# Optimization experiments

Hardware: AMD Instinct MI355X
Metric: run time of the kernel (lower is better)

Reference implementation:

```python
import jax, jax.numpy as jnp
import numpy as np

N_USERS = 100000
N_MOVIES = 20000
E = 2_000_000
D = 64          # in_units
F = 4           # num_factor
C = 5           # num_classes
H = 64          # hidden width of the edge MLP


def setup_inputs() -> dict:
    key = jax.random.key(0)
    ks = jax.random.split(key, 7)
    return {
        "ufeat": jax.random.normal(ks[0], (N_USERS, D), dtype=jnp.float32),
        "ifeat": jax.random.normal(ks[1], (N_MOVIES, D), dtype=jnp.float32),
        "W1": jax.random.normal(ks[2], (2 * D, H), dtype=jnp.float32) * 0.05,
        "W2": jax.random.normal(ks[3], (H, H), dtype=jnp.float32) * 0.05,
        "Wp": jax.random.normal(ks[4], (H, C), dtype=jnp.float32) * 0.05,
        "src_idx": jax.random.randint(ks[5], (E,), 0, N_USERS, dtype=jnp.int64) if jax.config.jax_enable_x64 else jax.random.randint(ks[5], (E,), 0, N_USERS, dtype=jnp.int32),
        "dst_idx": jax.random.randint(ks[6], (E,), 0, N_MOVIES, dtype=jnp.int32),
    }


def reference(ufeat, ifeat, W1, W2, Wp, src_idx, dst_idx):
    # Gather per-edge endpoint features (irregular access)
    h_u = ufeat[src_idx]   # [E, D]
    h_v = ifeat[dst_idx]   # [E, D]
    d = D // F
    # num_factor > 1 path: per-factor concat [h_u_k, h_v_k], then flatten.
    # Equivalent vectorized form: interleave factor blocks of u and v.
    x = jnp.concatenate(
        [h_u.reshape(-1, F, d), h_v.reshape(-1, F, d)], axis=2
    ).reshape(-1, 2 * D)   # [E, 2D]
    # Bias-free MLP: Linear -> exact GELU -> Linear (dropout rate is 0.0)
    h_fea = jax.nn.gelu(x @ W1, approximate=False) @ W2   # [E, 64]
    score = h_fea @ Wp                                    # [E, C] (squeeze is a no-op for C>1)
    return score, h_fea
```

## Files before the change

### kernel.cpp

```cpp
#include <hip/hip_runtime.h>
#include <hip/hip_bf16.h>

typedef short bf16x8 __attribute__((ext_vector_type(8)));
typedef float f32x4 __attribute__((ext_vector_type(4)));

#define E_TOTAL 2000000
#define MT 64
#define NTILES (E_TOTAL / MT)
#define NBLK (NTILES / 2)

#define NU 100000
#define NV 20000
#define NBU ((NU + 63) / 64)
#define NBV ((NV + 63) / 64)

#define OFF_W1UG 0
#define OFF_W1VG 4096
#define OFF_B2G  8192
#define OFF_U1   16384
#define OFF_V1   (16384 + 6400000)
#define WS_NEEDED_BYTES ((size_t)(OFF_V1 + 1280000) * 2)

#define FB_XP 136
#define FB_GP 72

__device__ __forceinline__ unsigned short f2bf(float x) {
  __hip_bfloat16 h = __float2bfloat16(x);
  return __builtin_bit_cast(unsigned short, h);
}
__device__ __forceinline__ float bf2f(unsigned short u) {
  unsigned int v = ((unsigned int)u) << 16;
  return __builtin_bit_cast(float, v);
}
__device__ __forceinline__ float gelu_exact(float x) {
  return 0.5f * x * (1.0f + erff(x * 0.70710678118654752f));
}
__device__ __forceinline__ float gelu_fast(float x) {
  float x2 = x * x;
  float inner = __builtin_fmaf(0.044715f * x, x2, x);
  float e = __builtin_amdgcn_exp2f(inner * 2.3022081f);
  float r = __builtin_amdgcn_rcpf(e + 1.0f);
  return __builtin_fmaf(-x, r, x);
}

__global__ void prep_w(const float* __restrict__ W1, const float* __restrict__ W2,
                       const float* __restrict__ Wp, unsigned short* __restrict__ ws) {
  int t = blockIdx.x * blockDim.x + threadIdx.x;
  int stride = gridDim.x * blockDim.x;
  unsigned short* W1ug = ws + OFF_W1UG;
  unsigned short* W1vg = ws + OFF_W1VG;
  unsigned short* B2g  = ws + OFF_B2G;
  for (int i = t; i < 4096; i += stride) {
    int n = i >> 6, k = i & 63;
    int xc = 32 * (k >> 4) + (k & 15);
    W1ug[i] = f2bf(W1[xc * 64 + n]);
    W1vg[i] = f2bf(W1[(xc + 16) * 64 + n]);
  }
  for (int i = t; i < 80 * 64; i += stride) {
    int n = i >> 6, k = i & 63;
    float v;
    if (n < 64) {
      v = W2[k * 64 + n];
    } else if (n < 69) {
      int c = n - 64;
      float s = 0.f;
      for (int j = 0; j < 64; ++j) s += W2[k * 64 + j] * Wp[j * 5 + c];
      v = s;
    } else {
      v = 0.f;
    }
    B2g[i] = f2bf(v);
  }
}

__global__ __launch_bounds__(256)
void prep_uv(const float* __restrict__ ufeat, const float* __restrict__ ifeat,
             const unsigned short* __restrict__ ws, unsigned short* __restrict__ wsmut) {
  const bool isU = (blockIdx.x < NBU);
  const int rows0 = (isU ? blockIdx.x : blockIdx.x - NBU) * 64;
  const int nrows = isU ? NU : NV;
  const float* feat = isU ? ufeat : ifeat;
  const unsigned short* Wg = ws + (isU ? OFF_W1UG : OFF_W1VG);
  unsigned short* outp = wsmut + (isU ? OFF_U1 : OFF_V1);

  const int lane = threadIdx.x & 63;
  const int w    = threadIdx.x >> 6;
  const int lr   = lane & 15;
  const int q    = lane >> 4;

  int row = rows0 + w * 16 + lr;
  int rowc = row < nrows ? row : nrows - 1;

  const f32x4 fz = {0.f, 0.f, 0.f, 0.f};
  f32x4 acc[4] = {fz, fz, fz, fz};
  #pragma unroll
  for (int kk = 0; kk < 2; ++kk) {
    int k0 = kk * 32 + q * 8;
    float4 fa = *reinterpret_cast<const float4*>(feat + (size_t)rowc * 64 + k0);
    float4 fb = *reinterpret_cast<const float4*>(feat + (size_t)rowc * 64 + k0 + 4);
    bf16x8 a;
    a[0] = (short)f2bf(fa.x); a[1] = (short)f2bf(fa.y);
    a[2] = (short)f2bf(fa.z); a[3] = (short)f2bf(fa.w);
    a[4] = (short)f2bf(fb.x); a[5] = (short)f2bf(fb.y);
    a[6] = (short)f2bf(fb.z); a[7] = (short)f2bf(fb.w);
    #pragma unroll
    for (int nt = 0; nt < 4; ++nt) {
      bf16x8 b = *reinterpret_cast<const bf16x8*>(&Wg[(nt * 16 + lr) * 64 + k0]);
      acc[nt] = __builtin_amdgcn_mfma_f32_16x16x32_bf16(b, a, acc[nt], 0, 0, 0);
    }
  }
  if (row < nrows) {
    #pragma unroll
    for (int nt = 0; nt < 4; ++nt) {
      ushort4 p;
      p.x = f2bf(acc[nt][0]); p.y = f2bf(acc[nt][1]);
      p.z = f2bf(acc[nt][2]); p.w = f2bf(acc[nt][3]);
      *reinterpret_cast<ushort4*>(&outp[(size_t)row * 64 + nt * 16 + 4 * q]) = p;
    }
  }
}

__device__ __forceinline__ void tile_compute(
    const unsigned short* __restrict__ B2g,
    bf16x8 u0, bf16x8 u1, bf16x8 v0, bf16x8 v1,
    int tbase, int w, int lr, int q, float* __restrict__ out) {
  const f32x4 fz = {0.f, 0.f, 0.f, 0.f};
  f32x4 acc[5] = {fz, fz, fz, fz, fz};
  bf16x8 g0, g1;
  #pragma unroll
  for (int e = 0; e < 8; ++e) {
    float x = bf2f((unsigned short)u0[e]) + bf2f((unsigned short)v0[e]);
    g0[e] = (short)f2bf(gelu_fast(x));
  }
  #pragma unroll
  for (int e = 0; e < 8; ++e) {
    float y = bf2f((unsigned short)u1[e]) + bf2f((unsigned short)v1[e]);
    g1[e] = (short)f2bf(gelu_fast(y));
  }
  const int k0 = q * 8;
  #pragma unroll
  for (int nt = 0; nt < 5; ++nt) {
    bf16x8 b0 = *reinterpret_cast<const bf16x8*>(&B2g[(nt * 16 + lr) * 64 + k0]);
    bf16x8 b1 = *reinterpret_cast<const bf16x8*>(&B2g[(nt * 16 + lr) * 64 + 32 + k0]);
    acc[nt] = __builtin_amdgcn_mfma_f32_16x16x32_bf16(b0, g0, acc[nt], 0, 0, 0);
    acc[nt] = __builtin_amdgcn_mfma_f32_16x16x32_bf16(b1, g1, acc[nt], 0, 0, 0);
  }
  float* out_score = out;
  float* out_h     = out + 10000000;
  const size_t edge = (size_t)(tbase + w * 16 + lr);
  #pragma unroll
  for (int nt = 0; nt < 4; ++nt)
    __builtin_nontemporal_store(acc[nt],
        reinterpret_cast<f32x4*>(&out_h[edge * 64 + nt * 16 + 4 * q]));
  if (q == 0) {
    *reinterpret_cast<f32x4*>(&out_score[edge * 5]) = acc[4];
  } else if (q == 1) {
    out_score[edge * 5 + 4] = acc[4][0];
  }
}

__global__ __launch_bounds__(256, 5)
void mlp_main5(const unsigned short* __restrict__ ws,
               const int* __restrict__ src, const int* __restrict__ dst,
               float* __restrict__ out) {
  const unsigned short* U1  = ws + OFF_U1;
  const unsigned short* V1  = ws + OFF_V1;
  const unsigned short* B2g = ws + OFF_B2G;

  const int lane = threadIdx.x & 63;
  const int w    = threadIdx.x >> 6;
  const int lr   = lane & 15;
  const int q    = lane >> 4;

  const int tb = blockIdx.x * (2 * MT);
  const int eA = tb + w * 16 + lr;
  const int eB = eA + 64;

  const int iA0 = src[eA];
  const int iA1 = dst[eA];
  const int iB0 = src[eB];
  const int iB1 = dst[eB];

  const unsigned short* upA = U1 + (size_t)iA0 * 64 + q * 8;
  const unsigned short* vpA = V1 + (size_t)iA1 * 64 + q * 8;
  const unsigned short* upB = U1 + (size_t)iB0 * 64 + q * 8;
  const unsigned short* vpB = V1 + (size_t)iB1 * 64 + q * 8;

  bf16x8 uA0 = *reinterpret_cast<const bf16x8*>(upA);
  bf16x8 uA1 = *reinterpret_cast<const bf16x8*>(upA + 32);
  bf16x8 vA0 = *reinterpret_cast<const bf16x8*>(vpA);
  bf16x8 vA1 = *reinterpret_cast<const bf16x8*>(vpA + 32);
  bf16x8 uB0 = *reinterpret_cast<const bf16x8*>(upB);
  bf16x8 uB1 = *reinterpret_cast<const bf16x8*>(upB + 32);
  bf16x8 vB0 = *reinterpret_cast<const bf16x8*>(vpB);
  bf16x8 vB1 = *reinterpret_cast<const bf16x8*>(vpB + 32);

  tile_compute(B2g, uA0, uA1, vA0, vA1, tb,      w, lr, q, out);
  tile_compute(B2g, uB0, uB1, vB0, vB1, tb + 64, w, lr, q, out);
}

__global__ void prep_kernel_fb(const float* __restrict__ W1, const float* __restrict__ W2,
                               const float* __restrict__ Wp,
                               unsigned short* __restrict__ W1g,
                               unsigned short* __restrict__ B2g) {
  int t = blockIdx.x * blockDim.x + threadIdx.x;
  int stride = gridDim.x * blockDim.x;
  for (int i = t; i < 64 * 128; i += stride) {
    int n = i >> 7, k = i & 127;
    W1g[i] = f2bf(W1[k * 64 + n]);
  }
  for (int i = t; i < 80 * 64; i += stride) {
    int n = i >> 6, k = i & 63;
    float v;
    if (n < 64) v = W2[k * 64 + n];
    else if (n < 69) {
      int c = n - 64; float s = 0.f;
      for (int j = 0; j < 64; ++j) s += W2[k * 64 + j] * Wp[j * 5 + c];
      v = s;
    } else v = 0.f;
    B2g[i] = f2bf(v);
  }
}

__global__ __launch_bounds__(256, 8)
void mlp_main_fb(const float* __restrict__ ufeat, const float* __restrict__ ifeat,
                 const int* __restrict__ src, const int* __restrict__ dst,
                 const unsigned short* __restrict__ W1g, const unsigned short* __restrict__ B2g,
                 float* __restrict__ out) {
  __shared__ __align__(16) unsigned short Xb[MT * FB_XP];
  const int lid  = threadIdx.x;
  const int lane = lid & 63;
  const int w    = lid >> 6;
  const int lr   = lane & 15;
  const int q    = lane >> 4;
  const int lk   = q << 3;
  const int tbase = blockIdx.x * MT;
  const int c  = lid & 15;
  const int rb = lid >> 4;
  int eidx[8];
  #pragma unroll
  for (int j = 0; j < 8; ++j) {
    int r = rb + 16 * j;
    eidx[j] = (r < 64) ? src[tbase + r] : dst[tbase + r - 64];
  }
  #pragma unroll
  for (int j = 0; j < 8; ++j) {
    int r = rb + 16 * j;
    int half = r >> 6;
    int e = r & 63;
    const float* base = (half ? ifeat : ufeat) + (size_t)eidx[j] * 64 + c * 4;
    float4 f = *reinterpret_cast<const float4*>(base);
    int col = ((c >> 2) * 32) + half * 16 + ((c & 3) * 4);
    ushort4 p;
    p.x = f2bf(f.x); p.y = f2bf(f.y); p.z = f2bf(f.z); p.w = f2bf(f.w);
    *reinterpret_cast<ushort4*>(&Xb[e * FB_XP + col]) = p;
  }
  __syncthreads();
  const f32x4 fz = {0.f, 0.f, 0.f, 0.f};
  f32x4 acc1[4] = {fz, fz, fz, fz};
  {
    const unsigned short* Xr = &Xb[(w * 16 + lr) * FB_XP];
    #pragma unroll
    for (int kk = 0; kk < 4; ++kk) {
      int ko = kk * 32 + lk;
      bf16x8 a = *reinterpret_cast<const bf16x8*>(Xr + ko);
      #pragma unroll
      for (int nt = 0; nt < 4; ++nt) {
        bf16x8 b = *reinterpret_cast<const bf16x8*>(&W1g[(nt * 16 + lr) * 128 + ko]);
        acc1[nt] = __builtin_amdgcn_mfma_f32_16x16x32_bf16(a, b, acc1[nt], 0, 0, 0);
      }
    }
  }
  __syncthreads();
  unsigned short* g = Xb;
  #pragma unroll
  for (int nt = 0; nt < 4; ++nt) {
    f32x4 v = acc1[nt];
    #pragma unroll
    for (int r = 0; r < 4; ++r)
      g[(w * 16 + 4 * q + r) * FB_GP + nt * 16 + lr] = f2bf(gelu_exact(v[r]));
  }
  __syncthreads();
  f32x4 acc2[5] = {fz, fz, fz, fz, fz};
  #pragma unroll
  for (int kk = 0; kk < 2; ++kk) {
    int ko = kk * 32 + lk;
    bf16x8 a = *reinterpret_cast<const bf16x8*>(&g[(w * 16 + lr) * FB_GP + ko]);
    #pragma unroll
    for (int nt = 0; nt < 5; ++nt) {
      bf16x8 b = *reinterpret_cast<const bf16x8*>(&B2g[(nt * 16 + lr) * 64 + ko]);
      acc2[nt] = __builtin_amdgcn_mfma_f32_16x16x32_bf16(a, b, acc2[nt], 0, 0, 0);
    }
  }
  float* out_score = out;
  float* out_h     = out + 10000000;
  {
    int er0 = tbase + w * 16 + 4 * q;
    #pragma unroll
    for (int nt = 0; nt < 4; ++nt) {
      #pragma unroll
      for (int r = 0; r < 4; ++r)
        out_h[(size_t)(er0 + r) * 64 + nt * 16 + lr] = acc2[nt][r];
    }
    if (lr < 5) {
      #pragma unroll
      for (int r = 0; r < 4; ++r)
        out_score[(size_t)(er0 + r) * 5 + lr] = acc2[4][r];
    }
  }
}

extern "C" void kernel_launch(void* const* d_in, const int* in_sizes, int n_in,
                              void* d_out, int out_size, void* d_ws, size_t ws_size,
                              hipStream_t stream) {
  const float* ufeat = (const float*)d_in[0];
  const float* ifeat = (const float*)d_in[1];
  const float* W1    = (const float*)d_in[2];
  const float* W2    = (const float*)d_in[3];
  const float* Wp    = (const float*)d_in[4];
  const int*   src   = (const int*)d_in[5];
  const int*   dst   = (const int*)d_in[6];

  unsigned short* ws = (unsigned short*)d_ws;

  if (ws_size >= WS_NEEDED_BYTES) {
    prep_w<<<16, 256, 0, stream>>>(W1, W2, Wp, ws);
    prep_uv<<<NBU + NBV, 256, 0, stream>>>(ufeat, ifeat, ws, ws);
    mlp_main5<<<NBLK, 256, 0, stream>>>(ws, src, dst, (float*)d_out);
  } else {
    unsigned short* W1g = ws;
    unsigned short* B2g = ws + 8192;
    prep_kernel_fb<<<16, 256, 0, stream>>>(W1, W2, Wp, W1g, B2g);
    mlp_main_fb<<<NTILES, 256, 0, stream>>>(ufeat, ifeat, src, dst, W1g, B2g, (float*)d_out);
  }
}
```

Measured before the change: 191.1 us.

## Convert main kernel to persistent grid with software-pipelined gathers

Replaces the one-shot kernel, where each block handles two tiles, with a persistent grid of 1024 blocks that loop over tiles in a grid stride. Each block keeps the W2/Wp weight fragments in registers and prefetches indices two tiles ahead and gathered features one tile ahead, so gather latency overlaps with GELU, MFMA and stores. The occupancy hint drops from 5 to 4 to make room for the extra live registers. With fewer waves resident, there is less latency hiding from oversubscription, and the clamped prefetch near the end does redundant loads.

```diff
diff --git a/kernel.cpp b/kernel.cpp
--- a/kernel.cpp
+++ b/kernel.cpp
@@ -7,7 +7,7 @@
 #define E_TOTAL 2000000
 #define MT 64
 #define NTILES (E_TOTAL / MT)
-#define NBLK (NTILES / 2)
+#define PGRID 1024
 
 #define NU 100000
 #define NV 20000
@@ -120,10 +120,32 @@
   }
 }
 
-__device__ __forceinline__ void tile_compute(
-    const unsigned short* __restrict__ B2g,
+struct Idx2 { int i0, i1; };
+
+__device__ __forceinline__ void idx_load(Idx2& ix, int tile, const int* __restrict__ src,
+                                         const int* __restrict__ dst, int elane) {
+  int e = tile * MT + elane;
+  ix.i0 = src[e];
+  ix.i1 = dst[e];
+}
+
+__device__ __forceinline__ void gather4(bf16x8& u0, bf16x8& u1, bf16x8& v0, bf16x8& v1,
+                                        const Idx2& ix,
+                                        const unsigned short* __restrict__ U1,
+                                        const unsigned short* __restrict__ V1, int q8) {
+  const unsigned short* up = U1 + (size_t)ix.i0 * 64 + q8;
+  const unsigned short* vp = V1 + (size_t)ix.i1 * 64 + q8;
+  u0 = *reinterpret_cast<const bf16x8*>(up);
+  u1 = *reinterpret_cast<const bf16x8*>(up + 32);
+  v0 = *reinterpret_cast<const bf16x8*>(vp);
+  v1 = *reinterpret_cast<const bf16x8*>(vp + 32);
+}
+
+__device__ __forceinline__ void compute_store(
+    const bf16x8 b2lo[5], const bf16x8 b2hi[5],
     bf16x8 u0, bf16x8 u1, bf16x8 v0, bf16x8 v1,
-    int tbase, int w, int lr, int q, float* __restrict__ out) {
+    int tile, int w, int lr, int q,
+    float* __restrict__ out_h, float* __restrict__ out_score) {
   const f32x4 fz = {0.f, 0.f, 0.f, 0.f};
   f32x4 acc[5] = {fz, fz, fz, fz, fz};
   bf16x8 g0, g1;
@@ -137,17 +159,12 @@
     float y = bf2f((unsigned short)u1[e]) + bf2f((unsigned short)v1[e]);
     g1[e] = (short)f2bf(gelu_fast(y));
   }
-  const int k0 = q * 8;
   #pragma unroll
   for (int nt = 0; nt < 5; ++nt) {
-    bf16x8 b0 = *reinterpret_cast<const bf16x8*>(&B2g[(nt * 16 + lr) * 64 + k0]);
-    bf16x8 b1 = *reinterpret_cast<const bf16x8*>(&B2g[(nt * 16 + lr) * 64 + 32 + k0]);
-    acc[nt] = __builtin_amdgcn_mfma_f32_16x16x32_bf16(b0, g0, acc[nt], 0, 0, 0);
-    acc[nt] = __builtin_amdgcn_mfma_f32_16x16x32_bf16(b1, g1, acc[nt], 0, 0, 0);
-  }
-  float* out_score = out;
-  float* out_h     = out + 10000000;
-  const size_t edge = (size_t)(tbase + w * 16 + lr);
+    acc[nt] = __builtin_amdgcn_mfma_f32_16x16x32_bf16(b2lo[nt], g0, acc[nt], 0, 0, 0);
+    acc[nt] = __builtin_amdgcn_mfma_f32_16x16x32_bf16(b2hi[nt], g1, acc[nt], 0, 0, 0);
+  }
+  const size_t edge = (size_t)(tile * MT + w * 16 + lr);
   #pragma unroll
   for (int nt = 0; nt < 4; ++nt)
     __builtin_nontemporal_store(acc[nt],
@@ -159,8 +176,8 @@
   }
 }
 
-__global__ __launch_bounds__(256, 5)
-void mlp_main5(const unsigned short* __restrict__ ws,
+__global__ __launch_bounds__(256, 4)
+void mlp_main6(const unsigned short* __restrict__ ws,
                const int* __restrict__ src, const int* __restrict__ dst,
                float* __restrict__ out) {
   const unsigned short* U1  = ws + OFF_U1;
@@ -171,32 +188,43 @@
   const int w    = threadIdx.x >> 6;
   const int lr   = lane & 15;
   const int q    = lane >> 4;
-
-  const int tb = blockIdx.x * (2 * MT);
-  const int eA = tb + w * 16 + lr;
-  const int eB = eA + 64;
-
-  const int iA0 = src[eA];
-  const int iA1 = dst[eA];
-  const int iB0 = src[eB];
-  const int iB1 = dst[eB];
-
-  const unsigned short* upA = U1 + (size_t)iA0 * 64 + q * 8;
-  const unsigned short* vpA = V1 + (size_t)iA1 * 64 + q * 8;
-  const unsigned short* upB = U1 + (size_t)iB0 * 64 + q * 8;
-  const unsigned short* vpB = V1 + (size_t)iB1 * 64 + q * 8;
-
-  bf16x8 uA0 = *reinterpret_cast<const bf16x8*>(upA);
-  bf16x8 uA1 = *reinterpret_cast<const bf16x8*>(upA + 32);
-  bf16x8 vA0 = *reinterpret_cast<const bf16x8*>(vpA);
-  bf16x8 vA1 = *reinterpret_cast<const bf16x8*>(vpA + 32);
-  bf16x8 uB0 = *reinterpret_cast<const bf16x8*>(upB);
-  bf16x8 uB1 = *reinterpret_cast<const bf16x8*>(upB + 32);
-  bf16x8 vB0 = *reinterpret_cast<const bf16x8*>(vpB);
-  bf16x8 vB1 = *reinterpret_cast<const bf16x8*>(vpB + 32);
-
-  tile_compute(B2g, uA0, uA1, vA0, vA1, tb,      w, lr, q, out);
-  tile_compute(B2g, uB0, uB1, vB0, vB1, tb + 64, w, lr, q, out);
+  const int q8   = q * 8;
+  const int elane = w * 16 + lr;
+
+  float* out_score = out;
+  float* out_h     = out + 10000000;
+
+  bf16x8 b2lo[5], b2hi[5];
+  #pragma unroll
+  for (int nt = 0; nt < 5; ++nt) {
+    b2lo[nt] = *reinterpret_cast<const bf16x8*>(&B2g[(nt * 16 + lr) * 64 + q8]);
+    b2hi[nt] = *reinterpret_cast<const bf16x8*>(&B2g[(nt * 16 + lr) * 64 + 32 + q8]);
+  }
+
+  Idx2 ia, ib;
+  bf16x8 ua0, ua1, va0, va1, ub0, ub1, vb0, vb1;
+
+  int t = blockIdx.x;
+  int t1 = t + PGRID;     if (t1 > NTILES - 1) t1 = NTILES - 1;
+  idx_load(ia, t,  src, dst, elane);
+  idx_load(ib, t1, src, dst, elane);
+  gather4(ua0, ua1, va0, va1, ia, U1, V1, q8);
+
+  bool useA = true;
+  for (; t < NTILES; t += PGRID) {
+    int t2 = t + 2 * PGRID;
+    if (t2 > NTILES - 1) t2 = NTILES - 1;
+    if (useA) {
+      idx_load(ia, t2, src, dst, elane);
+      gather4(ub0, ub1, vb0, vb1, ib, U1, V1, q8);
+      compute_store(b2lo, b2hi, ua0, ua1, va0, va1, t, w, lr, q, out_h, out_score);
+    } else {
+      idx_load(ib, t2, src, dst, elane);
+      gather4(ua0, ua1, va0, va1, ia, U1, V1, q8);
+      compute_store(b2lo, b2hi, ub0, ub1, vb0, vb1, t, w, lr, q, out_h, out_score);
+    }
+    useA = !useA;
+  }
 }
 
 __global__ void prep_kernel_fb(const float* __restrict__ W1, const float* __restrict__ W2,
@@ -326,7 +354,7 @@
   if (ws_size >= WS_NEEDED_BYTES) {
     prep_w<<<16, 256, 0, stream>>>(W1, W2, Wp, ws);
     prep_uv<<<NBU + NBV, 256, 0, stream>>>(ufeat, ifeat, ws, ws);
-    mlp_main5<<<NBLK, 256, 0, stream>>>(ws, src, dst, (float*)d_out);
+    mlp_main6<<<PGRID, 256, 0, stream>>>(ws, src, dst, (float*)d_out);
   } else {
     unsigned short* W1g = ws;
     unsigned short* B2g = ws + 8192;
```

Measured after the change: 198.1 us. +3.7%, slower.

## Bucket edges by source-user slice to improve gather cache locality

Applied to the files above, without the earlier changes.

Adds a histogram, scan and scatter pass that groups edges into 16 buckets by source-user range and packs each edge's index, src and dst into one 64-bit record. The main MLP kernel then processes edges bucket by bucket, with the block-to-bucket mapping interleaved, so the U1 table gathers hit a smaller working set in L2/MALL. Outputs are scattered back to the original edge positions. The extra passes read src/dst twice and write and read a 16 MB list, so they add traffic and launches. Per-bucket capacity is clamped, which would silently drop edges if a bucket overflowed; tails are handled with masked stores.

```diff
diff --git a/kernel.cpp b/kernel.cpp
--- a/kernel.cpp
+++ b/kernel.cpp
@@ -3,23 +3,32 @@
 
 typedef short bf16x8 __attribute__((ext_vector_type(8)));
 typedef float f32x4 __attribute__((ext_vector_type(4)));
+typedef unsigned long long u64;
 
 #define E_TOTAL 2000000
 #define MT 64
 #define NTILES (E_TOTAL / MT)
-#define NBLK (NTILES / 2)
 
 #define NU 100000
 #define NV 20000
 #define NBU ((NU + 63) / 64)
 #define NBV ((NV + 63) / 64)
+
+#define NBKT 16
+#define USLICE 6250u
+#define CAP16 262144
+#define BPB 2048
 
 #define OFF_W1UG 0
 #define OFF_W1VG 4096
 #define OFF_B2G  8192
 #define OFF_U1   16384
 #define OFF_V1   (16384 + 6400000)
-#define WS_NEEDED_BYTES ((size_t)(OFF_V1 + 1280000) * 2)
+#define LIST_B   15392768u
+#define HIST_B   (LIST_B + 33554432u)
+#define OFFS_B   (HIST_B + 16384u)
+#define CNTS_B   (OFFS_B + 16384u)
+#define WS_NEEDED_BYTES ((size_t)CNTS_B + 64)
 
 #define FB_XP 136
 #define FB_GP 72
@@ -120,10 +129,55 @@
   }
 }
 
+__global__ __launch_bounds__(256)
+void hist_k(const int* __restrict__ src, unsigned int* __restrict__ hist) {
+  __shared__ unsigned int c[NBKT];
+  if (threadIdx.x < NBKT) c[threadIdx.x] = 0;
+  __syncthreads();
+  for (int i = blockIdx.x * 256 + threadIdx.x; i < E_TOTAL; i += 256 * 256)
+    atomicAdd(&c[(unsigned)src[i] / USLICE], 1u);
+  __syncthreads();
+  if (threadIdx.x < NBKT) hist[blockIdx.x * NBKT + threadIdx.x] = c[threadIdx.x];
+}
+
+__global__ __launch_bounds__(256)
+void scan_k(const unsigned int* __restrict__ hist, unsigned int* __restrict__ offs,
+            unsigned int* __restrict__ cnts) {
+  __shared__ unsigned int h[256 * NBKT];
+  for (int i = threadIdx.x; i < 256 * NBKT; i += 256) h[i] = hist[i];
+  __syncthreads();
+  if (threadIdx.x < NBKT) {
+    unsigned run = 0;
+    for (int b = 0; b < 256; ++b) {
+      unsigned t = h[b * NBKT + threadIdx.x];
+      h[b * NBKT + threadIdx.x] = run;
+      run += t;
+    }
+    cnts[threadIdx.x] = run;
+  }
+  __syncthreads();
+  for (int i = threadIdx.x; i < 256 * NBKT; i += 256) offs[i] = h[i];
+}
+
+__global__ __launch_bounds__(256)
+void scat_k(const int* __restrict__ src, const int* __restrict__ dst,
+            const unsigned int* __restrict__ offs, u64* __restrict__ list) {
+  __shared__ unsigned int cur[NBKT];
+  if (threadIdx.x < NBKT) cur[threadIdx.x] = offs[blockIdx.x * NBKT + threadIdx.x];
+  __syncthreads();
+  for (int i = blockIdx.x * 256 + threadIdx.x; i < E_TOTAL; i += 256 * 256) {
+    unsigned s = (unsigned)src[i], d = (unsigned)dst[i];
+    unsigned b = s / USLICE;
+    unsigned slot = atomicAdd(&cur[b], 1u);
+    if (slot >= CAP16) slot = CAP16 - 1;
+    list[(size_t)b * CAP16 + slot] = (u64)i | ((u64)s << 21) | ((u64)d << 38);
+  }
+}
+
 __device__ __forceinline__ void tile_compute(
     const unsigned short* __restrict__ B2g,
     bf16x8 u0, bf16x8 u1, bf16x8 v0, bf16x8 v1,
-    int tbase, int w, int lr, int q, float* __restrict__ out) {
+    int edge, bool valid, int lr, int q, float* __restrict__ out) {
   const f32x4 fz = {0.f, 0.f, 0.f, 0.f};
   f32x4 acc[5] = {fz, fz, fz, fz, fz};
   bf16x8 g0, g1;
@@ -145,46 +199,65 @@
     acc[nt] = __builtin_amdgcn_mfma_f32_16x16x32_bf16(b0, g0, acc[nt], 0, 0, 0);
     acc[nt] = __builtin_amdgcn_mfma_f32_16x16x32_bf16(b1, g1, acc[nt], 0, 0, 0);
   }
-  float* out_score = out;
-  float* out_h     = out + 10000000;
-  const size_t edge = (size_t)(tbase + w * 16 + lr);
-  #pragma unroll
-  for (int nt = 0; nt < 4; ++nt)
-    __builtin_nontemporal_store(acc[nt],
-        reinterpret_cast<f32x4*>(&out_h[edge * 64 + nt * 16 + 4 * q]));
-  if (q == 0) {
-    *reinterpret_cast<f32x4*>(&out_score[edge * 5]) = acc[4];
-  } else if (q == 1) {
-    out_score[edge * 5 + 4] = acc[4][0];
-  }
-}
-
-__global__ __launch_bounds__(256, 5)
-void mlp_main5(const unsigned short* __restrict__ ws,
-               const int* __restrict__ src, const int* __restrict__ dst,
+  if (valid) {
+    float* out_score = out;
+    float* out_h     = out + 10000000;
+    const size_t e = (size_t)edge;
+    #pragma unroll
+    for (int nt = 0; nt < 4; ++nt)
+      __builtin_nontemporal_store(acc[nt],
+          reinterpret_cast<f32x4*>(&out_h[e * 64 + nt * 16 + 4 * q]));
+    if (q == 0) {
+      *reinterpret_cast<f32x4*>(&out_score[e * 5]) = acc[4];
+    } else if (q == 1) {
+      out_score[e * 5 + 4] = acc[4][0];
+    }
+  }
+}
+
+__global__ __launch_bounds__(256, 4)
+void mlp_main8(const unsigned short* __restrict__ ws,
+               const u64* __restrict__ list, const unsigned int* __restrict__ cnts,
                float* __restrict__ out) {
   const unsigned short* U1  = ws + OFF_U1;
   const unsigned short* V1  = ws + OFF_V1;
   const unsigned short* B2g = ws + OFF_B2G;
 
+  const int half = blockIdx.x >> 14;
+  const int sub  = blockIdx.x & 16383;
+  const int k    = half * 8 + (sub & 7);
+  const int j    = sub >> 3;
+
+  unsigned cnt = cnts[k];
+  if (cnt > CAP16) cnt = CAP16;
+  const int s0 = j * 128;
+  if (s0 >= (int)cnt) return;
+
   const int lane = threadIdx.x & 63;
   const int w    = threadIdx.x >> 6;
   const int lr   = lane & 15;
   const int q    = lane >> 4;
-
-  const int tb = blockIdx.x * (2 * MT);
-  const int eA = tb + w * 16 + lr;
-  const int eB = eA + 64;
-
-  const int iA0 = src[eA];
-  const int iA1 = dst[eA];
-  const int iB0 = src[eB];
-  const int iB1 = dst[eB];
-
-  const unsigned short* upA = U1 + (size_t)iA0 * 64 + q * 8;
-  const unsigned short* vpA = V1 + (size_t)iA1 * 64 + q * 8;
-  const unsigned short* upB = U1 + (size_t)iB0 * 64 + q * 8;
-  const unsigned short* vpB = V1 + (size_t)iB1 * 64 + q * 8;
+  const int q8   = q * 8;
+
+  const u64* L = list + (size_t)k * CAP16;
+  const int sA = s0 + w * 16 + lr;
+  const int sB = sA + 64;
+  const bool vA = sA < (int)cnt;
+  const bool vB = sB < (int)cnt;
+  u64 recA = L[vA ? sA : (int)cnt - 1];
+  u64 recB = L[vB ? sB : (int)cnt - 1];
+
+  const int eA  = (int)(recA & 0x1FFFFF);
+  const int iA0 = (int)((recA >> 21) & 0x1FFFF);
+  const int iA1 = (int)(recA >> 38);
+  const int eB  = (int)(recB & 0x1FFFFF);
+  const int iB0 = (int)((recB >> 21) & 0x1FFFF);
+  const int iB1 = (int)(recB >> 38);
+
+  const unsigned short* upA = U1 + (size_t)iA0 * 64 + q8;
+  const unsigned short* vpA = V1 + (size_t)iA1 * 64 + q8;
+  const unsigned short* upB = U1 + (size_t)iB0 * 64 + q8;
+  const unsigned short* vpB = V1 + (size_t)iB1 * 64 + q8;
 
   bf16x8 uA0 = *reinterpret_cast<const bf16x8*>(upA);
   bf16x8 uA1 = *reinterpret_cast<const bf16x8*>(upA + 32);
@@ -195,8 +268,8 @@
   bf16x8 vB0 = *reinterpret_cast<const bf16x8*>(vpB);
   bf16x8 vB1 = *reinterpret_cast<const bf16x8*>(vpB + 32);
 
-  tile_compute(B2g, uA0, uA1, vA0, vA1, tb,      w, lr, q, out);
-  tile_compute(B2g, uB0, uB1, vB0, vB1, tb + 64, w, lr, q, out);
+  tile_compute(B2g, uA0, uA1, vA0, vA1, eA, vA, lr, q, out);
+  tile_compute(B2g, uB0, uB1, vB0, vB1, eB, vB, lr, q, out);
 }
 
 __global__ void prep_kernel_fb(const float* __restrict__ W1, const float* __restrict__ W2,
@@ -324,9 +397,17 @@
   unsigned short* ws = (unsigned short*)d_ws;
 
   if (ws_size >= WS_NEEDED_BYTES) {
+    u64*          list = (u64*)((char*)d_ws + LIST_B);
+    unsigned int* hist = (unsigned int*)((char*)d_ws + HIST_B);
+    unsigned int* offs = (unsigned int*)((char*)d_ws + OFFS_B);
+    unsigned int* cnts = (unsigned int*)((char*)d_ws + CNTS_B);
+
     prep_w<<<16, 256, 0, stream>>>(W1, W2, Wp, ws);
     prep_uv<<<NBU + NBV, 256, 0, stream>>>(ufeat, ifeat, ws, ws);
-    mlp_main5<<<NBLK, 256, 0, stream>>>(ws, src, dst, (float*)d_out);
+    hist_k<<<256, 256, 0, stream>>>(src, hist);
+    scan_k<<<1, 256, 0, stream>>>(hist, offs, cnts);
+    scat_k<<<256, 256, 0, stream>>>(src, dst, offs, list);
+    mlp_main8<<<NBKT * BPB, 256, 0, stream>>>(ws, list, cnts, (float*)d_out);
   } else {
     unsigned short* W1g = ws;
     unsigned short* B2g = ws + 8192;
```

Measured after the change: 228.3 us, median of 2. 19.5% more time.
